# Optimization experiments

Measured on AMD Instinct MI355X. Metric: run time of the kernel, lower is better.

The kernel has to match this reference:

```python
import jax, jax.numpy as jnp
import numpy as np

B, S, D, H = 2, 2048, 1024, 16
HD = D // H

def setup_inputs() -> dict:
    key = jax.random.key(0)
    ks = jax.random.split(key, 9)
    s = 1.0 / np.sqrt(D)
    return {
        "x": jax.random.normal(ks[0], (B, S, D), jnp.float32),
        "Wq": jax.random.normal(ks[1], (D, D), jnp.float32) * s,
        "bq": jnp.zeros((D,), jnp.float32),
        "Wk": jax.random.normal(ks[2], (D, D), jnp.float32) * s,
        "bk": jnp.zeros((D,), jnp.float32),
        "Wv": jax.random.normal(ks[3], (D, D), jnp.float32) * s,
        "bv": jnp.zeros((D,), jnp.float32),
        "Wo": jax.random.normal(ks[4], (D, D), jnp.float32) * s,
        "bo": jnp.zeros((D,), jnp.float32),
    }

def reference(x, Wq, bq, Wk, bk, Wv, bv, Wo, bo):
    b, s, d = x.shape
    def split_heads(t):
        return t.reshape(b, s, H, HD).transpose(0, 2, 1, 3)  # [B,H,S,HD]
    q = split_heads(x @ Wq + bq)
    k = split_heads(x @ Wk + bk)
    v = split_heads(x @ Wv + bv)
    scores = jnp.einsum('bhqd,bhkd->bhqk', q, k) / jnp.sqrt(jnp.float32(HD))
    causal = jnp.tril(jnp.ones((s, s), bool))  # True = keep
    scores = jnp.where(causal, scores, -jnp.inf)
    attn = jax.nn.softmax(scores, axis=-1)
    out = jnp.einsum('bhqk,bhkd->bhqd', attn, v)  # [B,H,S,HD]
    out = out.transpose(0, 2, 1, 3).reshape(b, s, d)
    return out @ Wo + bo
```

## Files before the change

kernel.cpp:

```cpp
#include <hip/hip_runtime.h>

typedef unsigned short u16;
typedef unsigned int u32;
typedef __attribute__((ext_vector_type(8))) short bf16x8;
typedef __attribute__((ext_vector_type(4))) float f32x4;
typedef __attribute__((ext_vector_type(16))) float f32x16;

#define BB 2
#define SS 2048
#define DD 1024
#define HH 16
#define HD 64
#define MM (BB * SS)

__device__ inline float u2f(u32 u) { return __uint_as_float(u); }
__device__ inline u16 f2bf(float f) {
  u32 u = __float_as_uint(f);
  return (u16)((u + 0x7fffu + ((u >> 16) & 1u)) >> 16);
}

typedef const __attribute__((address_space(1))) void* gas_ptr;
typedef __attribute__((address_space(3))) void* las_ptr;
__device__ __forceinline__ void gll16(const void* g, void* l) {
  __builtin_amdgcn_global_load_lds((gas_ptr)g, (las_ptr)l, 16, 0, 0);
}

__device__ __forceinline__ u32 pk2(float a, float b) {
  return (__float_as_uint(a) >> 16) | (__float_as_uint(b) & 0xffff0000u);
}

__global__ __launch_bounds__(256) void prep(const float* __restrict__ x, u16* __restrict__ xb,
                                            const float* __restrict__ W0, const float* __restrict__ W1,
                                            const float* __restrict__ W2, const float* __restrict__ W3,
                                            u16* __restrict__ Wt) {
  int z = blockIdx.z;
  int t = threadIdx.x;
  if (z >= 4) {
    int gid = (z - 4) * 256 + blockIdx.y * 16 + blockIdx.x;
    int i = (gid * 256 + t) * 8;
    float4 a = *(const float4*)(x + i);
    float4 b = *(const float4*)(x + i + 4);
    uint4 o;
    o.x = (u32)f2bf(a.x) | ((u32)f2bf(a.y) << 16);
    o.y = (u32)f2bf(a.z) | ((u32)f2bf(a.w) << 16);
    o.z = (u32)f2bf(b.x) | ((u32)f2bf(b.y) << 16);
    o.w = (u32)f2bf(b.z) | ((u32)f2bf(b.w) << 16);
    *(uint4*)(xb + i) = o;
    return;
  }
  const float* W = (z == 0) ? W0 : (z == 1) ? W1 : (z == 2) ? W2 : W3;
  u16* out = Wt + (size_t)z * (DD * DD);
  __shared__ __align__(16) u16 T[64][72];
  int n0 = blockIdx.x * 64, k0 = blockIdx.y * 64;
#pragma unroll
  for (int p = 0; p < 4; ++p) {
    int kr = (t >> 4) + p * 16;
    int c4 = (t & 15) * 4;
    float4 v = *(const float4*)&W[(size_t)(k0 + kr) * DD + n0 + c4];
    T[c4 + 0][kr] = f2bf(v.x);
    T[c4 + 1][kr] = f2bf(v.y);
    T[c4 + 2][kr] = f2bf(v.z);
    T[c4 + 3][kr] = f2bf(v.w);
  }
  __syncthreads();
#pragma unroll
  for (int p = 0; p < 2; ++p) {
    int n = (t >> 3) + p * 32;
    int c8 = (t & 7) * 8;
    uint4 v = *(const uint4*)&T[n][c8];
    *(uint4*)&out[(size_t)(n0 + n) * DD + k0 + c8] = v;
  }
}

__global__ __launch_bounds__(256, 3) void gemm_qkv(const u16* __restrict__ xb, const u16* __restrict__ Wt,
                                                   const float* __restrict__ bq, const float* __restrict__ bk,
                                                   const float* __restrict__ bv,
                                                   u16* __restrict__ Qb, u16* __restrict__ Kb, u16* __restrict__ Vtb) {
  __shared__ __align__(16) u16 As[3 * 4096];
  __shared__ __align__(16) u16 Bs[3 * 4096];
  const int tid = threadIdx.x, lane = tid & 63, wv = tid >> 6;
  const int wm = (wv >> 1) * 64, wn = (wv & 1) * 64;
  const int l16 = lane & 15, quad = lane >> 4;

  const int id = blockIdx.x;
  const int xcd = id & 7, inner = id >> 3;
  const int mg = xcd >> 1, ng = xcd & 1;
  const int im = inner & 7, rest = inner >> 3;
  const int in_ = rest & 3, z = rest >> 2;
  const int m0 = (mg * 8 + im) * 128, n0 = (ng * 4 + in_) * 128;

  const u16* Bt = Wt + (size_t)z * (DD * DD);
  const float* bias = (z == 0) ? bq : (z == 1) ? bk : bv;

  const int r0 = tid >> 2, k8 = (tid & 3) << 3;
  const u16* Ap0 = &xb[(size_t)(m0 + r0) * DD + k8];
  const u16* Ap1 = Ap0 + (size_t)64 * DD;
  const u16* Bp0 = &Bt[(size_t)(n0 + r0) * DD + k8];
  const u16* Bp1 = Bp0 + (size_t)64 * DD;

  const int ldst = wv * 512;

#pragma unroll
  for (int p = 0; p < 3; ++p) {
    const int ko = p * 32, bo_ = p * 4096;
    gll16(Ap0 + ko, &As[bo_ + ldst]);
    gll16(Ap1 + ko, &As[bo_ + 2048 + ldst]);
    gll16(Bp0 + ko, &Bs[bo_ + ldst]);
    gll16(Bp1 + ko, &Bs[bo_ + 2048 + ldst]);
  }

  f32x4 acc[4][4];
  f32x4 zero = {0.f, 0.f, 0.f, 0.f};
#pragma unroll
  for (int i = 0; i < 4; ++i)
#pragma unroll
    for (int j = 0; j < 4; ++j) acc[i][j] = zero;

  asm volatile("s_waitcnt vmcnt(8)" ::: "memory");
  __builtin_amdgcn_s_barrier();

  int cur = 0;
  for (int t = 0; t < 32; ++t) {
    bf16x8 af[4], bg[4];
    const int cb = cur * 4096;
#pragma unroll
    for (int i = 0; i < 4; ++i) {
      af[i] = *(const bf16x8*)&As[cb + (wm + i * 16 + l16) * 32 + quad * 8];
      bg[i] = *(const bf16x8*)&Bs[cb + (wn + i * 16 + l16) * 32 + quad * 8];
    }
    asm volatile("s_waitcnt lgkmcnt(0)" ::: "memory");
    __builtin_amdgcn_s_barrier();
    if (t + 3 < 32) {
      const int ko = (t + 3) * 32;
      gll16(Ap0 + ko, &As[cb + ldst]);
      gll16(Ap1 + ko, &As[cb + 2048 + ldst]);
      gll16(Bp0 + ko, &Bs[cb + ldst]);
      gll16(Bp1 + ko, &Bs[cb + 2048 + ldst]);
    }
    __builtin_amdgcn_sched_barrier(0);
#pragma unroll
    for (int i = 0; i < 4; ++i)
#pragma unroll
      for (int j = 0; j < 4; ++j)
        acc[i][j] = __builtin_amdgcn_mfma_f32_16x16x32_bf16(af[i], bg[j], acc[i][j], 0, 0, 0);
    if (t <= 28)
      asm volatile("s_waitcnt vmcnt(8)" ::: "memory");
    else if (t == 29)
      asm volatile("s_waitcnt vmcnt(4)" ::: "memory");
    else if (t == 30)
      asm volatile("s_waitcnt vmcnt(0)" ::: "memory");
    if (t < 31) __builtin_amdgcn_s_barrier();
    cur = (cur == 2) ? 0 : cur + 1;
  }

  const float qsc = (z == 0) ? 0.180336880f : 1.0f;
  if (z == 2) {
#pragma unroll
    for (int i = 0; i < 4; ++i) {
#pragma unroll
      for (int j = 0; j < 4; ++j) {
        int col = n0 + wn + j * 16 + l16;
        float bcol = bias[col];
        int hh = col >> 6, dd = col & 63;
        int row0 = m0 + wm + i * 16;
        int bb = row0 >> 11, s0 = row0 & (SS - 1);
        int sbase = (s0 & ~63) + i * 16 + ((quad & 1) << 3) + ((quad >> 1) << 2);
        size_t base = (((size_t)((bb * HH + hh) * HD + dd)) << 11) + sbase;
        uint2 pv;
        pv.x = (u32)f2bf(acc[i][j][0] + bcol) | ((u32)f2bf(acc[i][j][1] + bcol) << 16);
        pv.y = (u32)f2bf(acc[i][j][2] + bcol) | ((u32)f2bf(acc[i][j][3] + bcol) << 16);
        *(uint2*)&Vtb[base] = pv;
      }
    }
  } else {
    u16* out = (z == 0) ? Qb : Kb;
#pragma unroll
    for (int i = 0; i < 4; ++i) {
#pragma unroll
      for (int j = 0; j < 4; ++j) {
        int col = n0 + wn + j * 16 + l16;
        float bcol = bias[col];
        int hh = col >> 6, dd = col & 63;
#pragma unroll
        for (int r = 0; r < 4; ++r) {
          int row = m0 + wm + i * 16 + quad * 4 + r;
          int bb = row >> 11, s = row & (SS - 1);
          out[((size_t)((bb * HH + hh) * SS + s) << 6) | dd] = f2bf((acc[i][j][r] + bcol) * qsc);
        }
      }
    }
  }
}

__global__ __launch_bounds__(256, 3) void gemm_out(const u16* __restrict__ Ub, const u16* __restrict__ Wot,
                                                   const float* __restrict__ bo, float* __restrict__ out) {
  __shared__ __align__(16) u16 As[3 * 4096];
  __shared__ __align__(16) u16 Bs[3 * 2048];
  const int tid = threadIdx.x, lane = tid & 63, wv = tid >> 6;
  const int wm = (wv >> 1) * 64, wn = (wv & 1) * 32;
  const int l16 = lane & 15, quad = lane >> 4;
  const int r0 = tid >> 2, k8 = (tid & 3) << 3;

  const int id = blockIdx.x;
  const int xcd = id & 7, inner = id >> 3;
  const int mg = xcd >> 1, ng = xcd & 1;
  const int im = inner & 7, in_ = inner >> 3;
  const int m0 = (mg * 8 + im) * 128, n0 = (ng * 8 + in_) * 64;

  const u16* Ap0 = &Ub[(size_t)(m0 + r0) * DD + k8];
  const u16* Ap1 = Ap0 + (size_t)64 * DD;
  const u16* Bp0 = &Wot[(size_t)(n0 + r0) * DD + k8];

  const int ldst = wv * 512;

#pragma unroll
  for (int p = 0; p < 3; ++p) {
    const int ko = p * 32;
    gll16(Ap0 + ko, &As[p * 4096 + ldst]);
    gll16(Ap1 + ko, &As[p * 4096 + 2048 + ldst]);
    gll16(Bp0 + ko, &Bs[p * 2048 + ldst]);
  }

  f32x4 acc[4][2];
  f32x4 zero = {0.f, 0.f, 0.f, 0.f};
#pragma unroll
  for (int i = 0; i < 4; ++i) { acc[i][0] = zero; acc[i][1] = zero; }

  asm volatile("s_waitcnt vmcnt(6)" ::: "memory");
  __builtin_amdgcn_s_barrier();

  int cur = 0;
  for (int t = 0; t < 32; ++t) {
    bf16x8 af[4], bg[2];
#pragma unroll
    for (int i = 0; i < 4; ++i) af[i] = *(const bf16x8*)&As[cur * 4096 + (wm + i * 16 + l16) * 32 + quad * 8];
#pragma unroll
    for (int j = 0; j < 2; ++j) bg[j] = *(const bf16x8*)&Bs[cur * 2048 + (wn + j * 16 + l16) * 32 + quad * 8];
    asm volatile("s_waitcnt lgkmcnt(0)" ::: "memory");
    __builtin_amdgcn_s_barrier();
    if (t + 3 < 32) {
      const int ko = (t + 3) * 32;
      gll16(Ap0 + ko, &As[cur * 4096 + ldst]);
      gll16(Ap1 + ko, &As[cur * 4096 + 2048 + ldst]);
      gll16(Bp0 + ko, &Bs[cur * 2048 + ldst]);
    }
    __builtin_amdgcn_sched_barrier(0);
#pragma unroll
    for (int i = 0; i < 4; ++i)
#pragma unroll
      for (int j = 0; j < 2; ++j)
        acc[i][j] = __builtin_amdgcn_mfma_f32_16x16x32_bf16(af[i], bg[j], acc[i][j], 0, 0, 0);
    if (t <= 28)
      asm volatile("s_waitcnt vmcnt(6)" ::: "memory");
    else if (t == 29)
      asm volatile("s_waitcnt vmcnt(3)" ::: "memory");
    else if (t == 30)
      asm volatile("s_waitcnt vmcnt(0)" ::: "memory");
    if (t < 31) __builtin_amdgcn_s_barrier();
    cur = (cur == 2) ? 0 : cur + 1;
  }

#pragma unroll
  for (int i = 0; i < 4; ++i) {
#pragma unroll
    for (int j = 0; j < 2; ++j) {
      int col = n0 + wn + j * 16 + l16;
      float bcol = bo[col];
#pragma unroll
      for (int r = 0; r < 4; ++r) {
        int row = m0 + wm + i * 16 + quad * 4 + r;
        out[(size_t)row * DD + col] = acc[i][j][r] + bcol;
      }
    }
  }
}

__global__ __launch_bounds__(256, 2) void attention_mfma(const u16* __restrict__ Q, const u16* __restrict__ K,
                                                         const u16* __restrict__ Vt, u16* __restrict__ Uo) {
  const int tid = threadIdx.x, lane = tid & 63, wv = tid >> 6;
  const int l31 = lane & 31, hi = lane >> 5;
  const int bh = blockIdx.x & 31;
  const int b = bh >> 4, h = bh & 15;
  const int g = blockIdx.x >> 5;
  const int qb = (blockIdx.x < 256) ? (15 - g) : (g - 8);
  const int q0 = qb * 128;
  const int qbase = q0 + wv * 32;
  const u16* Qh = Q + (size_t)(b * HH + h) * SS * HD;
  const u16* Kh = K + (size_t)(b * HH + h) * SS * HD;
  const u16* Vh = Vt + (size_t)(b * HH + h) * HD * SS;

  __shared__ __align__(16) u16 K_lds[2][4160];
  __shared__ __align__(16) u16 V_lds[2][4160];
  __shared__ float lsc[128];

  bf16x8 qf[4];
  {
    const u16* qp = &Qh[(size_t)(qbase + l31) * HD + 8 * hi];
#pragma unroll
    for (int m = 0; m < 4; ++m) qf[m] = *(const bf16x8*)(qp + 16 * m);
  }

  f32x16 o0, o1;
#pragma unroll
  for (int i = 0; i < 16; ++i) { o0[i] = 0.f; o1[i] = 0.f; }
  float lsum = 0.f;

  const int sr = tid >> 2, ci = tid & 3;
  const u16* Kg = &Kh[(size_t)sr * HD + ci * 8];
  const u16* Vg = &Vh[(size_t)sr * SS + ci * 8];
  const int ktiles = 2 * qb + 2;
  const int w0 = ci * 520 + sr * 8, w1 = (ci + 4) * 520 + sr * 8;

  uint4 ka = *(const uint4*)Kg, kb = *(const uint4*)(Kg + 32);
  uint4 va = *(const uint4*)Vg, vb = *(const uint4*)(Vg + 32);
  *(uint4*)&K_lds[0][w0] = ka;
  *(uint4*)&K_lds[0][w1] = kb;
  *(uint4*)&V_lds[0][w0] = va;
  *(uint4*)&V_lds[0][w1] = vb;
  {
    const u16* Kn = Kg + (size_t)64 * HD;
    const u16* Vn = Vg + 64;
    ka = *(const uint4*)Kn; kb = *(const uint4*)(Kn + 32);
    va = *(const uint4*)Vn; vb = *(const uint4*)(Vn + 32);
  }
  __syncthreads();

  for (int t = 0; t < ktiles; ++t) {
    const int cur = t & 1;
    if (64 * t <= qbase + 31) {
      f32x16 s0, s1;
#pragma unroll
      for (int i = 0; i < 16; ++i) { s0[i] = 0.f; s1[i] = 0.f; }
#pragma unroll
      for (int m = 0; m < 4; ++m) {
        const u16* kp = &K_lds[cur][(2 * m + hi) * 520 + l31 * 8];
        bf16x8 kf0 = *(const bf16x8*)kp;
        bf16x8 kf1 = *(const bf16x8*)(kp + 256);
        s0 = __builtin_amdgcn_mfma_f32_32x32x16_bf16(kf0, qf[m], s0, 0, 0, 0);
        s1 = __builtin_amdgcn_mfma_f32_32x32x16_bf16(kf1, qf[m], s1, 0, 0, 0);
      }
#pragma unroll
      for (int i = 0; i < 16; ++i) {
        s0[i] = __builtin_amdgcn_exp2f(s0[i]);
        s1[i] = __builtin_amdgcn_exp2f(s1[i]);
      }
      if (64 * t + 63 > qbase) {
        const int qq = qbase + l31, kb0 = 64 * t + 4 * hi;
#pragma unroll
        for (int p = 0; p < 4; ++p)
#pragma unroll
          for (int c = 0; c < 4; ++c) {
            if (kb0 + 8 * p + c > qq) s0[4 * p + c] = 0.f;
            if (kb0 + 32 + 8 * p + c > qq) s1[4 * p + c] = 0.f;
          }
      }
#pragma unroll
      for (int i = 0; i < 16; ++i) lsum += s0[i] + s1[i];

#pragma unroll
      for (int m = 0; m < 4; ++m) {
        const int p0 = 8 * (m & 1);
        union { uint4 u; bf16x8 v; } pa;
        if (m < 2) {
          pa.u.x = pk2(s0[p0 + 0], s0[p0 + 1]);
          pa.u.y = pk2(s0[p0 + 2], s0[p0 + 3]);
          pa.u.z = pk2(s0[p0 + 4], s0[p0 + 5]);
          pa.u.w = pk2(s0[p0 + 6], s0[p0 + 7]);
        } else {
          pa.u.x = pk2(s1[p0 + 0], s1[p0 + 1]);
          pa.u.y = pk2(s1[p0 + 2], s1[p0 + 3]);
          pa.u.z = pk2(s1[p0 + 4], s1[p0 + 5]);
          pa.u.w = pk2(s1[p0 + 6], s1[p0 + 7]);
        }
        const u16* vp = &V_lds[cur][(2 * m + hi) * 520 + l31 * 8];
        bf16x8 vf0 = *(const bf16x8*)vp;
        bf16x8 vf1 = *(const bf16x8*)(vp + 256);
        o0 = __builtin_amdgcn_mfma_f32_32x32x16_bf16(pa.v, vf0, o0, 0, 0, 0);
        o1 = __builtin_amdgcn_mfma_f32_32x32x16_bf16(pa.v, vf1, o1, 0, 0, 0);
      }
    }

    if (t + 1 < ktiles) {
      const int nxt = cur ^ 1;
      *(uint4*)&K_lds[nxt][w0] = ka;
      *(uint4*)&K_lds[nxt][w1] = kb;
      *(uint4*)&V_lds[nxt][w0] = va;
      *(uint4*)&V_lds[nxt][w1] = vb;
      if (t + 2 < ktiles) {
        const u16* Kn = Kg + (size_t)(t + 2) * 64 * HD;
        const u16* Vn = Vg + (t + 2) * 64;
        ka = *(const uint4*)Kn; kb = *(const uint4*)(Kn + 32);
        va = *(const uint4*)Vn; vb = *(const uint4*)(Vn + 32);
      }
    }
    __syncthreads();
  }

  lsum += __shfl_xor(lsum, 32);
  if (hi == 0) lsc[wv * 32 + l31] = 1.0f / lsum;
  __syncthreads();
  f32x4 lv[4];
#pragma unroll
  for (int p = 0; p < 4; ++p) lv[p] = *(const f32x4*)&lsc[wv * 32 + 8 * p + 4 * hi];

  u16* ub = Uo + (size_t)(b * SS) * DD + (h << 6);
#pragma unroll
  for (int p = 0; p < 4; ++p) {
#pragma unroll
    for (int c = 0; c < 4; ++c) {
      int row = qbase + 8 * p + 4 * hi + c;
      ub[(size_t)row * DD + l31] = f2bf(o0[4 * p + c] * lv[p][c]);
      ub[(size_t)row * DD + 32 + l31] = f2bf(o1[4 * p + c] * lv[p][c]);
    }
  }
}

extern "C" void kernel_launch(void* const* d_in, const int* in_sizes, int n_in,
                              void* d_out, int out_size, void* d_ws, size_t ws_size,
                              hipStream_t stream) {
  const float* x  = (const float*)d_in[0];
  const float* Wq = (const float*)d_in[1];
  const float* bq = (const float*)d_in[2];
  const float* Wk = (const float*)d_in[3];
  const float* bk = (const float*)d_in[4];
  const float* Wv = (const float*)d_in[5];
  const float* bv = (const float*)d_in[6];
  const float* Wo = (const float*)d_in[7];
  const float* bo = (const float*)d_in[8];
  float* out = (float*)d_out;

  char* ws = (char*)d_ws;
  u16* xb  = (u16*)(ws);
  u16* Wt  = (u16*)(ws + ((size_t)8 << 20));
  u16* Qb  = (u16*)(ws + ((size_t)16 << 20));
  u16* Kb  = (u16*)(ws + ((size_t)24 << 20));
  u16* Vtb = (u16*)(ws + ((size_t)32 << 20));
  u16* Ub  = (u16*)(ws + ((size_t)40 << 20));

  prep<<<dim3(16, 16, 12), dim3(256), 0, stream>>>(x, xb, Wq, Wk, Wv, Wo, Wt);
  gemm_qkv<<<dim3(768), dim3(256), 0, stream>>>(xb, Wt, bq, bk, bv, Qb, Kb, Vtb);
  attention_mfma<<<dim3(512), dim3(256), 0, stream>>>(Qb, Kb, Vtb, Ub);
  gemm_out<<<dim3(512), dim3(256), 0, stream>>>(Ub, Wt + (size_t)3 * DD * DD, bo, out);
}
```

Measured before the change: 167.8 us.

## Split attention key tiles across two wave groups with LDS reduction

The attention block grows from 4 to 8 waves. Each pair of waves shares the same 32 query rows but takes a different 32-key half of every 64-key tile, so each wave does half the QK and PV MFMAs per tile. Each K/V tile is loaded by a single thread group: half the threads stage K and half stage V. At the end, partial outputs and row sums from the second half are reduced through a 32 KB LDS buffer, which adds LDS use and extra barriers and may limit how many blocks fit per CU.

```diff
diff --git a/kernel.cpp b/kernel.cpp
--- a/kernel.cpp
+++ b/kernel.cpp
@@ -275,23 +275,25 @@
   }
 }
 
-__global__ __launch_bounds__(256, 2) void attention_mfma(const u16* __restrict__ Q, const u16* __restrict__ K,
+__global__ __launch_bounds__(512, 4) void attention_mfma(const u16* __restrict__ Q, const u16* __restrict__ K,
                                                          const u16* __restrict__ Vt, u16* __restrict__ Uo) {
   const int tid = threadIdx.x, lane = tid & 63, wv = tid >> 6;
   const int l31 = lane & 31, hi = lane >> 5;
+  const int kh = wv >> 2;
+  const int qw = wv & 3;
   const int bh = blockIdx.x & 31;
   const int b = bh >> 4, h = bh & 15;
   const int g = blockIdx.x >> 5;
   const int qb = (blockIdx.x < 256) ? (15 - g) : (g - 8);
-  const int q0 = qb * 128;
-  const int qbase = q0 + wv * 32;
+  const int qbase = qb * 128 + qw * 32;
   const u16* Qh = Q + (size_t)(b * HH + h) * SS * HD;
   const u16* Kh = K + (size_t)(b * HH + h) * SS * HD;
   const u16* Vh = Vt + (size_t)(b * HH + h) * HD * SS;
 
-  __shared__ __align__(16) u16 K_lds[2][4160];
-  __shared__ __align__(16) u16 V_lds[2][4160];
-  __shared__ float lsc[128];
+  __shared__ __align__(16) u16 KV[2][2][4160];
+  __shared__ float lsc1[128];
+  __shared__ float lsc0[128];
+  __shared__ float ored[4][2048];
 
   bf16x8 qf[4];
   {
@@ -305,112 +307,112 @@
   for (int i = 0; i < 16; ++i) { o0[i] = 0.f; o1[i] = 0.f; }
   float lsum = 0.f;
 
-  const int sr = tid >> 2, ci = tid & 3;
-  const u16* Kg = &Kh[(size_t)sr * HD + ci * 8];
-  const u16* Vg = &Vh[(size_t)sr * SS + ci * 8];
+  const int st = tid & 255;
+  const int sr = st >> 2, ci = st & 3;
+  const int kv = (tid < 256) ? 0 : 1;
+  const u16* Gp = (tid < 256) ? &Kh[(size_t)sr * HD + ci * 8] : &Vh[(size_t)sr * SS + ci * 8];
+  const int tstep = (tid < 256) ? 64 * HD : 64;
+  const int w0 = ci * 520 + sr * 8, w1 = (ci + 4) * 520 + sr * 8;
   const int ktiles = 2 * qb + 2;
-  const int w0 = ci * 520 + sr * 8, w1 = (ci + 4) * 520 + sr * 8;
-
-  uint4 ka = *(const uint4*)Kg, kb = *(const uint4*)(Kg + 32);
-  uint4 va = *(const uint4*)Vg, vb = *(const uint4*)(Vg + 32);
-  *(uint4*)&K_lds[0][w0] = ka;
-  *(uint4*)&K_lds[0][w1] = kb;
-  *(uint4*)&V_lds[0][w0] = va;
-  *(uint4*)&V_lds[0][w1] = vb;
+
+  uint4 a0 = *(const uint4*)Gp, a1 = *(const uint4*)(Gp + 32);
+  *(uint4*)&KV[0][kv][w0] = a0;
+  *(uint4*)&KV[0][kv][w1] = a1;
   {
-    const u16* Kn = Kg + (size_t)64 * HD;
-    const u16* Vn = Vg + 64;
-    ka = *(const uint4*)Kn; kb = *(const uint4*)(Kn + 32);
-    va = *(const uint4*)Vn; vb = *(const uint4*)(Vn + 32);
+    const u16* Gn = Gp + tstep;
+    a0 = *(const uint4*)Gn;
+    a1 = *(const uint4*)(Gn + 32);
   }
   __syncthreads();
 
   for (int t = 0; t < ktiles; ++t) {
     const int cur = t & 1;
-    if (64 * t <= qbase + 31) {
-      f32x16 s0, s1;
-#pragma unroll
-      for (int i = 0; i < 16; ++i) { s0[i] = 0.f; s1[i] = 0.f; }
+    const int k0 = 64 * t + 32 * kh;
+    if (k0 <= qbase + 31) {
+      f32x16 s;
+#pragma unroll
+      for (int i = 0; i < 16; ++i) s[i] = 0.f;
+      const int krow = (l31 + 32 * kh) * 8;
 #pragma unroll
       for (int m = 0; m < 4; ++m) {
-        const u16* kp = &K_lds[cur][(2 * m + hi) * 520 + l31 * 8];
-        bf16x8 kf0 = *(const bf16x8*)kp;
-        bf16x8 kf1 = *(const bf16x8*)(kp + 256);
-        s0 = __builtin_amdgcn_mfma_f32_32x32x16_bf16(kf0, qf[m], s0, 0, 0, 0);
-        s1 = __builtin_amdgcn_mfma_f32_32x32x16_bf16(kf1, qf[m], s1, 0, 0, 0);
-      }
-#pragma unroll
-      for (int i = 0; i < 16; ++i) {
-        s0[i] = __builtin_amdgcn_exp2f(s0[i]);
-        s1[i] = __builtin_amdgcn_exp2f(s1[i]);
-      }
-      if (64 * t + 63 > qbase) {
-        const int qq = qbase + l31, kb0 = 64 * t + 4 * hi;
+        const u16* kp = &KV[cur][0][(2 * m + hi) * 520 + krow];
+        s = __builtin_amdgcn_mfma_f32_32x32x16_bf16(*(const bf16x8*)kp, qf[m], s, 0, 0, 0);
+      }
+#pragma unroll
+      for (int i = 0; i < 16; ++i) s[i] = __builtin_amdgcn_exp2f(s[i]);
+      if (k0 + 31 > qbase) {
+        const int qq = qbase + l31, kb0 = k0 + 4 * hi;
 #pragma unroll
         for (int p = 0; p < 4; ++p)
 #pragma unroll
-          for (int c = 0; c < 4; ++c) {
-            if (kb0 + 8 * p + c > qq) s0[4 * p + c] = 0.f;
-            if (kb0 + 32 + 8 * p + c > qq) s1[4 * p + c] = 0.f;
-          }
-      }
-#pragma unroll
-      for (int i = 0; i < 16; ++i) lsum += s0[i] + s1[i];
-
-#pragma unroll
-      for (int m = 0; m < 4; ++m) {
-        const int p0 = 8 * (m & 1);
+          for (int c = 0; c < 4; ++c)
+            if (kb0 + 8 * p + c > qq) s[4 * p + c] = 0.f;
+      }
+#pragma unroll
+      for (int i = 0; i < 16; ++i) lsum += s[i];
+
+#pragma unroll
+      for (int m2 = 0; m2 < 2; ++m2) {
+        const int p0 = 8 * m2;
         union { uint4 u; bf16x8 v; } pa;
-        if (m < 2) {
-          pa.u.x = pk2(s0[p0 + 0], s0[p0 + 1]);
-          pa.u.y = pk2(s0[p0 + 2], s0[p0 + 3]);
-          pa.u.z = pk2(s0[p0 + 4], s0[p0 + 5]);
-          pa.u.w = pk2(s0[p0 + 6], s0[p0 + 7]);
-        } else {
-          pa.u.x = pk2(s1[p0 + 0], s1[p0 + 1]);
-          pa.u.y = pk2(s1[p0 + 2], s1[p0 + 3]);
-          pa.u.z = pk2(s1[p0 + 4], s1[p0 + 5]);
-          pa.u.w = pk2(s1[p0 + 6], s1[p0 + 7]);
-        }
-        const u16* vp = &V_lds[cur][(2 * m + hi) * 520 + l31 * 8];
-        bf16x8 vf0 = *(const bf16x8*)vp;
-        bf16x8 vf1 = *(const bf16x8*)(vp + 256);
-        o0 = __builtin_amdgcn_mfma_f32_32x32x16_bf16(pa.v, vf0, o0, 0, 0, 0);
-        o1 = __builtin_amdgcn_mfma_f32_32x32x16_bf16(pa.v, vf1, o1, 0, 0, 0);
+        pa.u.x = pk2(s[p0 + 0], s[p0 + 1]);
+        pa.u.y = pk2(s[p0 + 2], s[p0 + 3]);
+        pa.u.z = pk2(s[p0 + 4], s[p0 + 5]);
+        pa.u.w = pk2(s[p0 + 6], s[p0 + 7]);
+        const u16* vp = &KV[cur][1][(2 * (2 * kh + m2) + hi) * 520 + l31 * 8];
+        o0 = __builtin_amdgcn_mfma_f32_32x32x16_bf16(pa.v, *(const bf16x8*)vp, o0, 0, 0, 0);
+        o1 = __builtin_amdgcn_mfma_f32_32x32x16_bf16(pa.v, *(const bf16x8*)(vp + 256), o1, 0, 0, 0);
       }
     }
 
     if (t + 1 < ktiles) {
       const int nxt = cur ^ 1;
-      *(uint4*)&K_lds[nxt][w0] = ka;
-      *(uint4*)&K_lds[nxt][w1] = kb;
-      *(uint4*)&V_lds[nxt][w0] = va;
-      *(uint4*)&V_lds[nxt][w1] = vb;
+      *(uint4*)&KV[nxt][kv][w0] = a0;
+      *(uint4*)&KV[nxt][kv][w1] = a1;
       if (t + 2 < ktiles) {
-        const u16* Kn = Kg + (size_t)(t + 2) * 64 * HD;
-        const u16* Vn = Vg + (t + 2) * 64;
-        ka = *(const uint4*)Kn; kb = *(const uint4*)(Kn + 32);
-        va = *(const uint4*)Vn; vb = *(const uint4*)(Vn + 32);
+        const u16* Gn = Gp + (size_t)(t + 2) * tstep;
+        a0 = *(const uint4*)Gn;
+        a1 = *(const uint4*)(Gn + 32);
       }
     }
     __syncthreads();
   }
 
   lsum += __shfl_xor(lsum, 32);
-  if (hi == 0) lsc[wv * 32 + l31] = 1.0f / lsum;
+
+  if (kh == 1) {
+    if (hi == 0) lsc1[qw * 32 + l31] = lsum;
+#pragma unroll
+    for (int i = 0; i < 16; ++i) {
+      ored[qw][i * 64 + lane] = o0[i];
+      ored[qw][(16 + i) * 64 + lane] = o1[i];
+    }
+  }
   __syncthreads();
-  f32x4 lv[4];
-#pragma unroll
-  for (int p = 0; p < 4; ++p) lv[p] = *(const f32x4*)&lsc[wv * 32 + 8 * p + 4 * hi];
-
-  u16* ub = Uo + (size_t)(b * SS) * DD + (h << 6);
-#pragma unroll
-  for (int p = 0; p < 4; ++p) {
-#pragma unroll
-    for (int c = 0; c < 4; ++c) {
-      int row = qbase + 8 * p + 4 * hi + c;
-      ub[(size_t)row * DD + l31] = f2bf(o0[4 * p + c] * lv[p][c]);
-      ub[(size_t)row * DD + 32 + l31] = f2bf(o1[4 * p + c] * lv[p][c]);
+  if (kh == 0) {
+#pragma unroll
+    for (int i = 0; i < 16; ++i) {
+      o0[i] += ored[qw][i * 64 + lane];
+      o1[i] += ored[qw][(16 + i) * 64 + lane];
+    }
+    float tot = lsum + lsc1[qw * 32 + l31];
+    if (hi == 0) lsc0[qw * 32 + l31] = 1.0f / tot;
+  }
+  __syncthreads();
+  if (kh == 0) {
+    f32x4 lv[4];
+#pragma unroll
+    for (int p = 0; p < 4; ++p) lv[p] = *(const f32x4*)&lsc0[qw * 32 + 8 * p + 4 * hi];
+
+    u16* ub = Uo + (size_t)(b * SS) * DD + (h << 6);
+#pragma unroll
+    for (int p = 0; p < 4; ++p) {
+#pragma unroll
+      for (int c = 0; c < 4; ++c) {
+        int row = qbase + 8 * p + 4 * hi + c;
+        ub[(size_t)row * DD + l31] = f2bf(o0[4 * p + c] * lv[p][c]);
+        ub[(size_t)row * DD + 32 + l31] = f2bf(o1[4 * p + c] * lv[p][c]);
+      }
     }
   }
 }
@@ -439,6 +441,6 @@
 
   prep<<<dim3(16, 16, 12), dim3(256), 0, stream>>>(x, xb, Wq, Wk, Wv, Wo, Wt);
   gemm_qkv<<<dim3(768), dim3(256), 0, stream>>>(xb, Wt, bq, bk, bv, Qb, Kb, Vtb);
-  attention_mfma<<<dim3(512), dim3(256), 0, stream>>>(Qb, Kb, Vtb, Ub);
+  attention_mfma<<<dim3(512), dim3(512), 0, stream>>>(Qb, Kb, Vtb, Ub);
   gemm_out<<<dim3(512), dim3(256), 0, stream>>>(Ub, Wt + (size_t)3 * DD * DD, bo, out);
 }
```

Result: no change. 168.5 us (+0.4%).

## Split attention into 64-row query tiles with 2-wave blocks and balanced ordering

Applied to the files above, without the earlier changes.

The attention kernel now uses 128-thread blocks, each covering 64 query rows instead of 128, launched as 1024 blocks. Query tiles are ordered so that long causal tiles and short ones interleave, which should balance work across CUs. Each thread now loads four 16-byte K/V chunks per tile instead of two, and the per-wave skip of fully masked tiles is dropped because every K tile up to the diagonal is now needed by both waves. More blocks means more redundant K/V loading per query row, in exchange for finer-grained scheduling and less tail imbalance.

```diff
diff --git a/kernel.cpp b/kernel.cpp
--- a/kernel.cpp
+++ b/kernel.cpp
@@ -275,23 +275,23 @@
   }
 }
 
-__global__ __launch_bounds__(256, 2) void attention_mfma(const u16* __restrict__ Q, const u16* __restrict__ K,
+__global__ __launch_bounds__(128, 2) void attention_mfma(const u16* __restrict__ Q, const u16* __restrict__ K,
                                                          const u16* __restrict__ Vt, u16* __restrict__ Uo) {
   const int tid = threadIdx.x, lane = tid & 63, wv = tid >> 6;
   const int l31 = lane & 31, hi = lane >> 5;
   const int bh = blockIdx.x & 31;
   const int b = bh >> 4, h = bh & 15;
-  const int g = blockIdx.x >> 5;
-  const int qb = (blockIdx.x < 256) ? (15 - g) : (g - 8);
-  const int q0 = qb * 128;
-  const int qbase = q0 + wv * 32;
+  const int j = blockIdx.x >> 8;
+  const int g = (blockIdx.x >> 5) & 7;
+  const int qt = (j == 0) ? g : (j == 1) ? (15 - g) : (j == 2) ? (16 + g) : (31 - g);
+  const int qbase = qt * 64 + wv * 32;
   const u16* Qh = Q + (size_t)(b * HH + h) * SS * HD;
   const u16* Kh = K + (size_t)(b * HH + h) * SS * HD;
   const u16* Vh = Vt + (size_t)(b * HH + h) * HD * SS;
 
   __shared__ __align__(16) u16 K_lds[2][4160];
   __shared__ __align__(16) u16 V_lds[2][4160];
-  __shared__ float lsc[128];
+  __shared__ float lsc[64];
 
   bf16x8 qf[4];
   {
@@ -305,92 +305,98 @@
   for (int i = 0; i < 16; ++i) { o0[i] = 0.f; o1[i] = 0.f; }
   float lsum = 0.f;
 
-  const int sr = tid >> 2, ci = tid & 3;
-  const u16* Kg = &Kh[(size_t)sr * HD + ci * 8];
-  const u16* Vg = &Vh[(size_t)sr * SS + ci * 8];
-  const int ktiles = 2 * qb + 2;
-  const int w0 = ci * 520 + sr * 8, w1 = (ci + 4) * 520 + sr * 8;
-
-  uint4 ka = *(const uint4*)Kg, kb = *(const uint4*)(Kg + 32);
-  uint4 va = *(const uint4*)Vg, vb = *(const uint4*)(Vg + 32);
-  *(uint4*)&K_lds[0][w0] = ka;
-  *(uint4*)&K_lds[0][w1] = kb;
-  *(uint4*)&V_lds[0][w0] = va;
-  *(uint4*)&V_lds[0][w1] = vb;
+  const int sr = tid >> 1, c0 = (tid & 1) << 2;
+  const u16* Kg = &Kh[(size_t)sr * HD + c0 * 8];
+  const u16* Vg = &Vh[(size_t)sr * SS + c0 * 8];
+  const int ktiles = qt + 1;
+
+  uint4 kr[4], vr[4];
+#pragma unroll
+  for (int pp = 0; pp < 4; ++pp) {
+    kr[pp] = *(const uint4*)(Kg + pp * 8);
+    vr[pp] = *(const uint4*)(Vg + pp * 8);
+    *(uint4*)&K_lds[0][(c0 + pp) * 520 + sr * 8] = kr[pp];
+    *(uint4*)&V_lds[0][(c0 + pp) * 520 + sr * 8] = vr[pp];
+  }
   {
     const u16* Kn = Kg + (size_t)64 * HD;
     const u16* Vn = Vg + 64;
-    ka = *(const uint4*)Kn; kb = *(const uint4*)(Kn + 32);
-    va = *(const uint4*)Vn; vb = *(const uint4*)(Vn + 32);
+#pragma unroll
+    for (int pp = 0; pp < 4; ++pp) {
+      kr[pp] = *(const uint4*)(Kn + pp * 8);
+      vr[pp] = *(const uint4*)(Vn + pp * 8);
+    }
   }
   __syncthreads();
 
   for (int t = 0; t < ktiles; ++t) {
     const int cur = t & 1;
-    if (64 * t <= qbase + 31) {
-      f32x16 s0, s1;
-#pragma unroll
-      for (int i = 0; i < 16; ++i) { s0[i] = 0.f; s1[i] = 0.f; }
-#pragma unroll
-      for (int m = 0; m < 4; ++m) {
-        const u16* kp = &K_lds[cur][(2 * m + hi) * 520 + l31 * 8];
-        bf16x8 kf0 = *(const bf16x8*)kp;
-        bf16x8 kf1 = *(const bf16x8*)(kp + 256);
-        s0 = __builtin_amdgcn_mfma_f32_32x32x16_bf16(kf0, qf[m], s0, 0, 0, 0);
-        s1 = __builtin_amdgcn_mfma_f32_32x32x16_bf16(kf1, qf[m], s1, 0, 0, 0);
-      }
-#pragma unroll
-      for (int i = 0; i < 16; ++i) {
-        s0[i] = __builtin_amdgcn_exp2f(s0[i]);
-        s1[i] = __builtin_amdgcn_exp2f(s1[i]);
-      }
-      if (64 * t + 63 > qbase) {
-        const int qq = qbase + l31, kb0 = 64 * t + 4 * hi;
-#pragma unroll
-        for (int p = 0; p < 4; ++p)
-#pragma unroll
-          for (int c = 0; c < 4; ++c) {
-            if (kb0 + 8 * p + c > qq) s0[4 * p + c] = 0.f;
-            if (kb0 + 32 + 8 * p + c > qq) s1[4 * p + c] = 0.f;
-          }
-      }
-#pragma unroll
-      for (int i = 0; i < 16; ++i) lsum += s0[i] + s1[i];
-
-#pragma unroll
-      for (int m = 0; m < 4; ++m) {
-        const int p0 = 8 * (m & 1);
-        union { uint4 u; bf16x8 v; } pa;
-        if (m < 2) {
-          pa.u.x = pk2(s0[p0 + 0], s0[p0 + 1]);
-          pa.u.y = pk2(s0[p0 + 2], s0[p0 + 3]);
-          pa.u.z = pk2(s0[p0 + 4], s0[p0 + 5]);
-          pa.u.w = pk2(s0[p0 + 6], s0[p0 + 7]);
-        } else {
-          pa.u.x = pk2(s1[p0 + 0], s1[p0 + 1]);
-          pa.u.y = pk2(s1[p0 + 2], s1[p0 + 3]);
-          pa.u.z = pk2(s1[p0 + 4], s1[p0 + 5]);
-          pa.u.w = pk2(s1[p0 + 6], s1[p0 + 7]);
+    f32x16 s0, s1;
+#pragma unroll
+    for (int i = 0; i < 16; ++i) { s0[i] = 0.f; s1[i] = 0.f; }
+#pragma unroll
+    for (int m = 0; m < 4; ++m) {
+      const u16* kp = &K_lds[cur][(2 * m + hi) * 520 + l31 * 8];
+      bf16x8 kf0 = *(const bf16x8*)kp;
+      bf16x8 kf1 = *(const bf16x8*)(kp + 256);
+      s0 = __builtin_amdgcn_mfma_f32_32x32x16_bf16(kf0, qf[m], s0, 0, 0, 0);
+      s1 = __builtin_amdgcn_mfma_f32_32x32x16_bf16(kf1, qf[m], s1, 0, 0, 0);
+    }
+#pragma unroll
+    for (int i = 0; i < 16; ++i) {
+      s0[i] = __builtin_amdgcn_exp2f(s0[i]);
+      s1[i] = __builtin_amdgcn_exp2f(s1[i]);
+    }
+    if (64 * t + 63 > qbase) {
+      const int qq = qbase + l31, kb0 = 64 * t + 4 * hi;
+#pragma unroll
+      for (int p = 0; p < 4; ++p)
+#pragma unroll
+        for (int c = 0; c < 4; ++c) {
+          if (kb0 + 8 * p + c > qq) s0[4 * p + c] = 0.f;
+          if (kb0 + 32 + 8 * p + c > qq) s1[4 * p + c] = 0.f;
         }
-        const u16* vp = &V_lds[cur][(2 * m + hi) * 520 + l31 * 8];
-        bf16x8 vf0 = *(const bf16x8*)vp;
-        bf16x8 vf1 = *(const bf16x8*)(vp + 256);
-        o0 = __builtin_amdgcn_mfma_f32_32x32x16_bf16(pa.v, vf0, o0, 0, 0, 0);
-        o1 = __builtin_amdgcn_mfma_f32_32x32x16_bf16(pa.v, vf1, o1, 0, 0, 0);
-      }
+    }
+#pragma unroll
+    for (int i = 0; i < 16; ++i) lsum += s0[i] + s1[i];
+
+#pragma unroll
+    for (int m = 0; m < 4; ++m) {
+      const int p0 = 8 * (m & 1);
+      union { uint4 u; bf16x8 v; } pa;
+      if (m < 2) {
+        pa.u.x = pk2(s0[p0 + 0], s0[p0 + 1]);
+        pa.u.y = pk2(s0[p0 + 2], s0[p0 + 3]);
+        pa.u.z = pk2(s0[p0 + 4], s0[p0 + 5]);
+        pa.u.w = pk2(s0[p0 + 6], s0[p0 + 7]);
+      } else {
+        pa.u.x = pk2(s1[p0 + 0], s1[p0 + 1]);
+        pa.u.y = pk2(s1[p0 + 2], s1[p0 + 3]);
+        pa.u.z = pk2(s1[p0 + 4], s1[p0 + 5]);
+        pa.u.w = pk2(s1[p0 + 6], s1[p0 + 7]);
+      }
+      const u16* vp = &V_lds[cur][(2 * m + hi) * 520 + l31 * 8];
+      bf16x8 vf0 = *(const bf16x8*)vp;
+      bf16x8 vf1 = *(const bf16x8*)(vp + 256);
+      o0 = __builtin_amdgcn_mfma_f32_32x32x16_bf16(pa.v, vf0, o0, 0, 0, 0);
+      o1 = __builtin_amdgcn_mfma_f32_32x32x16_bf16(pa.v, vf1, o1, 0, 0, 0);
     }
 
     if (t + 1 < ktiles) {
       const int nxt = cur ^ 1;
-      *(uint4*)&K_lds[nxt][w0] = ka;
-      *(uint4*)&K_lds[nxt][w1] = kb;
-      *(uint4*)&V_lds[nxt][w0] = va;
-      *(uint4*)&V_lds[nxt][w1] = vb;
+#pragma unroll
+      for (int pp = 0; pp < 4; ++pp) {
+        *(uint4*)&K_lds[nxt][(c0 + pp) * 520 + sr * 8] = kr[pp];
+        *(uint4*)&V_lds[nxt][(c0 + pp) * 520 + sr * 8] = vr[pp];
+      }
       if (t + 2 < ktiles) {
         const u16* Kn = Kg + (size_t)(t + 2) * 64 * HD;
         const u16* Vn = Vg + (t + 2) * 64;
-        ka = *(const uint4*)Kn; kb = *(const uint4*)(Kn + 32);
-        va = *(const uint4*)Vn; vb = *(const uint4*)(Vn + 32);
+#pragma unroll
+        for (int pp = 0; pp < 4; ++pp) {
+          kr[pp] = *(const uint4*)(Kn + pp * 8);
+          vr[pp] = *(const uint4*)(Vn + pp * 8);
+        }
       }
     }
     __syncthreads();
@@ -439,6 +445,6 @@
 
   prep<<<dim3(16, 16, 12), dim3(256), 0, stream>>>(x, xb, Wq, Wk, Wv, Wo, Wt);
   gemm_qkv<<<dim3(768), dim3(256), 0, stream>>>(xb, Wt, bq, bk, bv, Qb, Kb, Vtb);
-  attention_mfma<<<dim3(512), dim3(256), 0, stream>>>(Qb, Kb, Vtb, Ub);
+  attention_mfma<<<dim3(1024), dim3(128), 0, stream>>>(Qb, Kb, Vtb, Ub);
   gemm_out<<<dim3(512), dim3(256), 0, stream>>>(Ub, Wt + (size_t)3 * DD * DD, bo, out);
 }
```

Result: slower. 223.3 us (+33.1%).
